# Optimization experiments

Measured on AMD Instinct MI355X. Metric: run time of the kernel, lower is better.

## Reference

```python
import jax, jax.numpy as jnp
import numpy as np

WH, WW = 7, 7            # window size
NUM_HEADS = 4
PROMPT_LEN = 20          # PERTASK_LEN(5) * 4 tasks
DIM = 128
HEAD_DIM = DIM // NUM_HEADS
SCALE = HEAD_DIM ** -0.5


def _relative_position_index(wh, ww):
    coords = np.stack(np.meshgrid(np.arange(wh), np.arange(ww), indexing='ij'))  # [2,wh,ww]
    cf = coords.reshape(2, -1)                               # [2, wh*ww]
    rc = (cf[:, :, None] - cf[:, None, :]).transpose(1, 2, 0).astype(np.int64)
    rc[..., 0] += wh - 1
    rc[..., 1] += ww - 1
    rc[..., 0] *= 2 * ww - 1
    return rc.sum(-1)                                        # [wh*ww, wh*ww]

_REL_IDX = jnp.asarray(_relative_position_index(WH, WW))


def setup_inputs() -> dict:
    key = jax.random.key(0)
    ks = jax.random.split(key, 8)
    B, nW = 32, 64
    B_ = B * nW
    Nw = WH * WW
    return {
        'x': jax.random.normal(ks[0], (B_, Nw, DIM), jnp.float32),
        'spa_prompts': jax.random.normal(ks[1], (B, PROMPT_LEN, DIM), jnp.float32),
        'mask': jax.random.normal(ks[2], (nW, Nw, Nw), jnp.float32),
        'rel_bias_table': jax.random.normal(ks[3], ((2 * WH - 1) * (2 * WW - 1), NUM_HEADS), jnp.float32) * 0.02,
        'W_qkv': jax.random.normal(ks[4], (DIM, 3 * DIM), jnp.float32) * 0.02,
        'b_qkv': jax.random.normal(ks[5], (3 * DIM,), jnp.float32) * 0.02,
        'W_proj': jax.random.normal(ks[6], (DIM, DIM), jnp.float32) * 0.02,
        'b_proj': jax.random.normal(ks[7], (DIM,), jnp.float32) * 0.02,
    }


def reference(x, spa_prompts, mask, rel_bias_table, W_qkv, b_qkv, W_proj, b_proj):
    B_, Nw, C = x.shape
    B = spa_prompts.shape[0]
    nW = B_ // B
    P = PROMPT_LEN
    H = NUM_HEADS

    # replicate prompts per window and concat in front of window tokens
    prompts = jnp.broadcast_to(spa_prompts[:, None], (B, nW, P, C)).reshape(B_, P, C)
    xc = jnp.concatenate([prompts, x], axis=1)               # [B_, N, C]
    N = P + Nw

    qkv = xc @ W_qkv + b_qkv                                 # [B_, N, 3C]
    qkv = qkv.reshape(B_, N, 3, H, HEAD_DIM).transpose(2, 0, 3, 1, 4)
    q, k, v = qkv[0], qkv[1], qkv[2]                         # [B_, H, N, hd]

    attn_w = jnp.einsum('bhnd,bhmd->bhnm', q, k)             # unscaled q@k^T
    attn = attn_w * SCALE

    # relative position bias on the window-token sub-block
    bias = rel_bias_table[_REL_IDX]                          # [Nw, Nw, H]
    bias = bias.transpose(2, 0, 1)                           # [H, Nw, Nw]
    attn = attn.at[:, :, P:, P:].add(bias[None])

    # shifted-window mask on the same sub-block
    attn = attn.reshape(B, nW, H, N, N)
    attn = attn.at[:, :, :, P:, P:].add(mask[None, :, None])
    attn = attn.reshape(B_, H, N, N)

    attn = jax.nn.softmax(attn, axis=-1)

    out = jnp.einsum('bhnm,bhmd->bhnd', attn, v)             # [B_, H, N, hd]
    out = out.transpose(0, 2, 1, 3).reshape(B_, N, C)
    out = out @ W_proj + b_proj

    prompts_out, x_out = out[:, :P, :], out[:, P:, :]
    prompts_out = prompts_out.reshape(B, nW, P, C).mean(axis=1)
    ori_attn_weight = attn_w[:, :, :P, P:]                   # prompt->token raw scores
    return x_out, ori_attn_weight, prompts_out
```

## Files before the change

### kernel.cpp

```cpp
#include <hip/hip_runtime.h>
#include <hip/hip_bf16.h>

#define B_TOT   2048
#define BGRP    32
#define NW      64
#define NWIN    49
#define PLEN    20
#define NTOK    69
#define CDIM    128
#define NH      4
#define HD      32
#define SCALE_F 0.17677669529663687f

#define WIN_ROWS (B_TOT * NWIN)
#define PROMPT_ROWS (BGRP * PLEN)
#define TOT_ROWS (WIN_ROWS + PROMPT_ROWS)
#define PROJ_ROWS (B_TOT * NTOK)

typedef unsigned short ushort_t;
typedef __attribute__((ext_vector_type(8))) short bf16x8;
typedef __attribute__((ext_vector_type(4))) float f32x4;

__device__ __forceinline__ ushort_t f2b(float f) {
    union { float f; unsigned u; } v; v.f = f;
    unsigned r = v.u + 0x7FFFu + ((v.u >> 16) & 1u);
    return (ushort_t)(r >> 16);
}

__global__ __launch_bounds__(256) void convw_kernel(
    const float* __restrict__ Wqkv, const float* __restrict__ Wproj,
    ushort_t* __restrict__ Wtq, ushort_t* __restrict__ Wtp)
{
    int idx = blockIdx.x * 256 + threadIdx.x;
    if (idx < 384 * 128) {
        int n = idx >> 7, k = idx & 127;
        Wtq[idx] = f2b(Wqkv[k * 384 + n]);
    } else {
        int i = idx - 384 * 128;
        int n = i >> 7, k = i & 127;
        Wtp[i] = f2b(Wproj[k * 128 + n]);
    }
}

__global__ __launch_bounds__(256) void bm_kernel(
    const float* __restrict__ relb, const float* __restrict__ mask, float* __restrict__ bm)
{
    int idx = blockIdx.x * 256 + threadIdx.x;
    int jj = idx % 49; int t = idx / 49; int ii = t % 49; int wh = t / 49;
    int h = wh & 3, w = wh >> 2;
    int ridx = (ii / 7 - jj / 7 + 6) * 13 + (ii % 7 - jj % 7 + 6);
    bm[idx] = relb[ridx * NH + h] + mask[((size_t)w * 49 + ii) * 49 + jj];
}

__global__ __launch_bounds__(256) void qkv_kernel(
    const float* __restrict__ x, const float* __restrict__ prompts,
    const ushort_t* __restrict__ Wtq, const float* __restrict__ bqkv,
    ushort_t* __restrict__ q_win, ushort_t* __restrict__ k_win, ushort_t* __restrict__ v_win,
    ushort_t* __restrict__ q_p, ushort_t* __restrict__ k_p, ushort_t* __restrict__ v_p)
{
    __shared__ __align__(16) ushort_t As[128][136];
    __shared__ __align__(16) ushort_t Bs[128][136];
    const int m0 = blockIdx.x * 128;
    const int by = blockIdx.y;
    const int tid = threadIdx.x;

    for (int it = tid; it < 128 * 16; it += 256) {
        int r = it >> 4, ch = it & 15;
        int row = m0 + r;
        const float* src = (row < WIN_ROWS) ? x + (size_t)row * CDIM + ch * 8
                                            : prompts + (size_t)(row - WIN_ROWS) * CDIM + ch * 8;
        float4 v0 = *(const float4*)src;
        float4 v1 = *(const float4*)(src + 4);
        ushort_t tmp[8] = {f2b(v0.x), f2b(v0.y), f2b(v0.z), f2b(v0.w),
                           f2b(v1.x), f2b(v1.y), f2b(v1.z), f2b(v1.w)};
        *(uint4*)&As[r][ch * 8] = *(uint4*)tmp;
    }
    for (int it = tid; it < 128 * 16; it += 256) {
        int r = it >> 4, ch = it & 15;
        *(uint4*)&Bs[r][ch * 8] = *(const uint4*)(Wtq + ((size_t)(by * 128 + r)) * 128 + ch * 8);
    }
    __syncthreads();

    const int lane = tid & 63, wv = tid >> 6;
    const int wr = wv >> 1, wc = wv & 1;
    const int c = lane & 15, quad = lane >> 4;

    f32x4 acc[4][4];
#pragma unroll
    for (int i = 0; i < 4; i++)
#pragma unroll
        for (int j = 0; j < 4; j++) acc[i][j] = (f32x4){0.f, 0.f, 0.f, 0.f};

#pragma unroll
    for (int kc = 0; kc < 4; kc++) {
        bf16x8 a[4], b[4];
#pragma unroll
        for (int i = 0; i < 4; i++) a[i] = *(const bf16x8*)&As[wr * 64 + i * 16 + c][kc * 32 + quad * 8];
#pragma unroll
        for (int j = 0; j < 4; j++) b[j] = *(const bf16x8*)&Bs[wc * 64 + j * 16 + c][kc * 32 + quad * 8];
#pragma unroll
        for (int i = 0; i < 4; i++)
#pragma unroll
            for (int j = 0; j < 4; j++)
                acc[i][j] = __builtin_amdgcn_mfma_f32_16x16x32_bf16(a[i], b[j], acc[i][j], 0, 0, 0);
    }

    ushort_t* dw = (by == 0) ? q_win : (by == 1) ? k_win : v_win;
    ushort_t* dp = (by == 0) ? q_p   : (by == 1) ? k_p   : v_p;
    const bool iswin = (m0 < WIN_ROWS);

#pragma unroll
    for (int j = 0; j < 4; j++) {
        int col = wc * 64 + j * 16 + c;
        float bias = bqkv[by * 128 + col];
        int h = col >> 5, d = col & 31;
#pragma unroll
        for (int i = 0; i < 4; i++) {
            int row0 = m0 + wr * 64 + i * 16 + quad * 4;
            if (iswin) {
                int bidx = row0 / 49, n = row0 - bidx * 49;
#pragma unroll
                for (int rr = 0; rr < 4; rr++) {
                    dw[(((size_t)bidx * NH + h) * NWIN + n) * HD + d] = f2b(acc[i][j][rr] + bias);
                    if (++n == 49) { n = 0; ++bidx; }
                }
            } else {
                int ir = row0 - WIN_ROWS;
                int bb2 = ir / 20, p = ir - bb2 * 20;
#pragma unroll
                for (int rr = 0; rr < 4; rr++) {
                    dp[(((size_t)bb2 * NH + h) * PLEN + p) * HD + d] = f2b(acc[i][j][rr] + bias);
                    if (++p == 20) { p = 0; ++bb2; }
                }
            }
        }
    }
}

__global__ __launch_bounds__(256) void attn_kernel(
    const ushort_t* __restrict__ q_win, const ushort_t* __restrict__ k_win, const ushort_t* __restrict__ v_win,
    const ushort_t* __restrict__ q_p, const ushort_t* __restrict__ k_p, const ushort_t* __restrict__ v_p,
    const float* __restrict__ bm,
    ushort_t* __restrict__ attn_out, float* __restrict__ ori_w)
{
    __shared__ __align__(16) ushort_t Qs[80][72];
    __shared__ __align__(16) ushort_t Ks[80][72];
    __shared__ __align__(16) ushort_t Vt[32][112];
    __shared__ __align__(16) ushort_t Ps[80][104];

    const int b = blockIdx.x >> 2;
    const int h = blockIdx.x & 3;
    const int bb = b >> 6;
    const int w = b & 63;
    const int tid = threadIdx.x;

    for (int it = tid; it < 69 * 4; it += 256) {
        int n = it >> 2, ch = it & 3;
        size_t o;
        const ushort_t *qb, *kb, *vb;
        if (n < PLEN) {
            o = (((size_t)bb * NH + h) * PLEN + n) * HD + ch * 8;
            qb = q_p; kb = k_p; vb = v_p;
        } else {
            o = (((size_t)b * NH + h) * NWIN + (n - PLEN)) * HD + ch * 8;
            qb = q_win; kb = k_win; vb = v_win;
        }
        *(uint4*)&Qs[n][ch * 8] = *(const uint4*)(qb + o);
        *(uint4*)&Ks[n][ch * 8] = *(const uint4*)(kb + o);
        uint4 vv = *(const uint4*)(vb + o);
        ushort_t tmp[8]; *(uint4*)tmp = vv;
#pragma unroll
        for (int d = 0; d < 8; d++) Vt[ch * 8 + d][n] = tmp[d];
    }
    for (int it = tid; it < 11 * 9 * 2; it += 256) {
        int which = it / 99, rem = it % 99;
        int r = 69 + rem / 9, ch = rem % 9;
        uint4 z = {0u, 0u, 0u, 0u};
        if (which == 0) *(uint4*)&Qs[r][ch * 8] = z;
        else            *(uint4*)&Ks[r][ch * 8] = z;
    }
    for (int it = tid; it < 32 * 27; it += 256) Vt[it / 27][69 + it % 27] = 0;
    for (int it = tid; it < 80 * 2; it += 256) {
        uint4 z = {0u, 0u, 0u, 0u};
        *(uint4*)&Ps[it >> 1][80 + (it & 1) * 8] = z;
    }
    __syncthreads();

    const int lane = tid & 63, wv = tid >> 6;
    const int c = lane & 15, quad = lane >> 4;
    const float* bmw = bm + (size_t)(w * NH + h) * (49 * 49);
    float* OtF = (float*)&Qs[0][0];

    for (int itile = wv; itile < 5; itile += 4) {
        bf16x8 aq = *(const bf16x8*)&Qs[itile * 16 + c][quad * 8];
        f32x4 s[5];
#pragma unroll
        for (int j = 0; j < 5; j++) {
            bf16x8 bk = *(const bf16x8*)&Ks[j * 16 + c][quad * 8];
            s[j] = __builtin_amdgcn_mfma_f32_16x16x32_bf16(aq, bk, (f32x4){0.f, 0.f, 0.f, 0.f}, 0, 0, 0);
        }
        const int mbase = itile * 16 + quad * 4;

        if (mbase < 20) {
#pragma unroll
            for (int j = 1; j < 5; j++) {
                int col = j * 16 + c;
                if (col >= 20 && col < 69) {
#pragma unroll
                    for (int rr = 0; rr < 4; rr++) {
                        int m = mbase + rr;
                        if (m < 20)
                            ori_w[(((size_t)b * NH + h) * PLEN + m) * NWIN + (col - 20)] = s[j][rr];
                    }
                }
            }
        }
#pragma unroll
        for (int j = 0; j < 5; j++) {
            int col = j * 16 + c;
#pragma unroll
            for (int rr = 0; rr < 4; rr++) {
                int m = mbase + rr;
                float v;
                if (col >= 69) v = -1e30f;
                else {
                    v = s[j][rr] * SCALE_F;
                    if (m >= 20 && m < 69 && col >= 20)
                        v += bmw[(m - 20) * 49 + (col - 20)];
                }
                s[j][rr] = v;
            }
        }
#pragma unroll
        for (int rr = 0; rr < 4; rr++) {
            float mx = s[0][rr];
#pragma unroll
            for (int j = 1; j < 5; j++) mx = fmaxf(mx, s[j][rr]);
            mx = fmaxf(mx, __shfl_xor(mx, 1));
            mx = fmaxf(mx, __shfl_xor(mx, 2));
            mx = fmaxf(mx, __shfl_xor(mx, 4));
            mx = fmaxf(mx, __shfl_xor(mx, 8));
            float e[5], sum = 0.f;
#pragma unroll
            for (int j = 0; j < 5; j++) { e[j] = __expf(s[j][rr] - mx); sum += e[j]; }
            sum += __shfl_xor(sum, 1);
            sum += __shfl_xor(sum, 2);
            sum += __shfl_xor(sum, 4);
            sum += __shfl_xor(sum, 8);
            float inv = 1.f / sum;
            int m = mbase + rr;
#pragma unroll
            for (int j = 0; j < 5; j++) Ps[m][j * 16 + c] = f2b(e[j] * inv);
        }
#pragma unroll
        for (int dt = 0; dt < 2; dt++) {
            f32x4 o = {0.f, 0.f, 0.f, 0.f};
#pragma unroll
            for (int kc = 0; kc < 3; kc++) {
                bf16x8 pa = *(const bf16x8*)&Ps[itile * 16 + c][kc * 32 + quad * 8];
                bf16x8 vb = *(const bf16x8*)&Vt[dt * 16 + c][kc * 32 + quad * 8];
                o = __builtin_amdgcn_mfma_f32_16x16x32_bf16(pa, vb, o, 0, 0, 0);
            }
#pragma unroll
            for (int rr = 0; rr < 4; rr++)
                OtF[(itile * 16 + quad * 4 + rr) * 36 + dt * 16 + c] = o[rr];
        }
    }
    __syncthreads();

    for (int it = tid; it < 69 * 8; it += 256) {
        int n = it >> 3, ch = it & 7;
        float4 ov = *(const float4*)&OtF[n * 36 + ch * 4];
        uint2 pk;
        pk.x = (unsigned)f2b(ov.x) | ((unsigned)f2b(ov.y) << 16);
        pk.y = (unsigned)f2b(ov.z) | ((unsigned)f2b(ov.w) << 16);
        *(uint2*)(attn_out + ((size_t)b * NTOK + n) * CDIM + h * HD + ch * 4) = pk;
    }
}

__global__ __launch_bounds__(256) void proj_kernel(
    const ushort_t* __restrict__ attn_out, const ushort_t* __restrict__ Wtp,
    const float* __restrict__ bproj,
    float* __restrict__ x_out, float* __restrict__ promptproj)
{
    __shared__ __align__(16) ushort_t As[128][136];
    __shared__ __align__(16) ushort_t Bs[128][136];
    const int m0 = blockIdx.x * 128;
    const int tid = threadIdx.x;

    for (int it = tid; it < 128 * 16; it += 256) {
        int r = it >> 4, ch = it & 15;
        *(uint4*)&As[r][ch * 8] = *(const uint4*)(attn_out + (size_t)(m0 + r) * CDIM + ch * 8);
    }
    for (int it = tid; it < 128 * 16; it += 256) {
        int r = it >> 4, ch = it & 15;
        *(uint4*)&Bs[r][ch * 8] = *(const uint4*)(Wtp + (size_t)r * 128 + ch * 8);
    }
    __syncthreads();

    const int lane = tid & 63, wv = tid >> 6;
    const int wr = wv >> 1, wc = wv & 1;
    const int c = lane & 15, quad = lane >> 4;

    f32x4 acc[4][4];
#pragma unroll
    for (int i = 0; i < 4; i++)
#pragma unroll
        for (int j = 0; j < 4; j++) acc[i][j] = (f32x4){0.f, 0.f, 0.f, 0.f};

#pragma unroll
    for (int kc = 0; kc < 4; kc++) {
        bf16x8 a[4], b[4];
#pragma unroll
        for (int i = 0; i < 4; i++) a[i] = *(const bf16x8*)&As[wr * 64 + i * 16 + c][kc * 32 + quad * 8];
#pragma unroll
        for (int j = 0; j < 4; j++) b[j] = *(const bf16x8*)&Bs[wc * 64 + j * 16 + c][kc * 32 + quad * 8];
#pragma unroll
        for (int i = 0; i < 4; i++)
#pragma unroll
            for (int j = 0; j < 4; j++)
                acc[i][j] = __builtin_amdgcn_mfma_f32_16x16x32_bf16(a[i], b[j], acc[i][j], 0, 0, 0);
    }

#pragma unroll
    for (int j = 0; j < 4; j++) {
        int col = wc * 64 + j * 16 + c;
        float bias = bproj[col];
#pragma unroll
        for (int i = 0; i < 4; i++) {
            int row0 = m0 + wr * 64 + i * 16 + quad * 4;
            int bidx = row0 / 69, n = row0 - bidx * 69;
#pragma unroll
            for (int rr = 0; rr < 4; rr++) {
                float val = acc[i][j][rr] + bias;
                if (n >= PLEN)
                    x_out[((size_t)bidx * NWIN + (n - PLEN)) * CDIM + col] = val;
                else
                    promptproj[((size_t)bidx * PLEN + n) * CDIM + col] = val;
                if (++n == 69) { n = 0; ++bidx; }
            }
        }
    }
}

__global__ __launch_bounds__(256) void mean_kernel(
    const float* __restrict__ promptproj, float* __restrict__ prompts_out)
{
    int idx = blockIdx.x * 256 + threadIdx.x;
    if (idx >= BGRP * PLEN * CDIM) return;
    int c = idx & 127;
    int p = (idx >> 7) % PLEN;
    int bb = idx / (PLEN * CDIM);
    size_t base = (((size_t)bb * NW) * PLEN + p) * CDIM + c;
    float s = 0.f;
    for (int w = 0; w < NW; w++) s += promptproj[base + (size_t)w * (PLEN * CDIM)];
    prompts_out[idx] = s * (1.f / 64.f);
}

extern "C" void kernel_launch(void* const* d_in, const int* in_sizes, int n_in,
                              void* d_out, int out_size, void* d_ws, size_t ws_size,
                              hipStream_t stream)
{
    const float* x       = (const float*)d_in[0];
    const float* prompts = (const float*)d_in[1];
    const float* mask    = (const float*)d_in[2];
    const float* relb    = (const float*)d_in[3];
    const float* Wqkv    = (const float*)d_in[4];
    const float* bqkv    = (const float*)d_in[5];
    const float* Wproj   = (const float*)d_in[6];
    const float* bproj   = (const float*)d_in[7];

    float* out = (float*)d_out;
    float* x_out       = out;
    float* ori_w       = out + (size_t)B_TOT * NWIN * CDIM;
    float* prompts_out = ori_w + (size_t)B_TOT * NH * PLEN * NWIN;

    char* wsb = (char*)d_ws;
    size_t off = 0;
    const size_t winQKV = (size_t)B_TOT * NH * NWIN * HD;
    const size_t pQKV   = (size_t)BGRP * NH * PLEN * HD;
    ushort_t* q_win = (ushort_t*)(wsb + off); off += winQKV * 2;
    ushort_t* k_win = (ushort_t*)(wsb + off); off += winQKV * 2;
    ushort_t* v_win = (ushort_t*)(wsb + off); off += winQKV * 2;
    ushort_t* q_p   = (ushort_t*)(wsb + off); off += pQKV * 2;
    ushort_t* k_p   = (ushort_t*)(wsb + off); off += pQKV * 2;
    ushort_t* v_p   = (ushort_t*)(wsb + off); off += pQKV * 2;
    ushort_t* attn_o = (ushort_t*)(wsb + off); off += (size_t)B_TOT * NTOK * CDIM * 2;
    float* promptproj = (float*)(wsb + off); off += (size_t)B_TOT * PLEN * CDIM * 4;
    float* bm = (float*)(wsb + off); off += (size_t)NW * NH * 49 * 49 * 4;
    ushort_t* Wtq = (ushort_t*)(wsb + off); off += 384 * 128 * 2;
    ushort_t* Wtp = (ushort_t*)(wsb + off); off += 128 * 128 * 2;

    convw_kernel<<<256, 256, 0, stream>>>(Wqkv, Wproj, Wtq, Wtp);
    bm_kernel<<<(NW * NH * 49 * 49) / 256, 256, 0, stream>>>(relb, mask, bm);
    qkv_kernel<<<dim3(TOT_ROWS / 128, 3), 256, 0, stream>>>(x, prompts, Wtq, bqkv,
                                                            q_win, k_win, v_win, q_p, k_p, v_p);
    attn_kernel<<<B_TOT * NH, 256, 0, stream>>>(q_win, k_win, v_win, q_p, k_p, v_p,
                                                bm, attn_o, ori_w);
    proj_kernel<<<PROJ_ROWS / 128, 256, 0, stream>>>(attn_o, Wtp, bproj, x_out, promptproj);
    mean_kernel<<<(BGRP * PLEN * CDIM + 255) / 256, 256, 0, stream>>>(promptproj, prompts_out);
}
```

Before: 306.2 us.

## Use token-major QKV layout, one block per window, and LDS-staged coalesced epilogues

The QKV GEMM now writes q/k/v in token-major [row][128] layout by staging its bf16 output tile in LDS and emitting 16-byte coalesced stores, replacing scattered per-element head-major writes. The attention kernel switches from one block per (window, head) to one block per window, with each wave handling one head. K and Q fragments are loaded straight from global into registers, and V is transposed once into LDS for all heads. The projection epilogue likewise stages fp32 results in LDS for vectorized float4 stores. This targets uncoalesced global writes and redundant loads, at the cost of each wave processing all five query tiles serially and more direct global reads inside the loop.

```diff
diff --git a/kernel.cpp b/kernel.cpp
--- a/kernel.cpp
+++ b/kernel.cpp
@@ -105,100 +105,99 @@
                 acc[i][j] = __builtin_amdgcn_mfma_f32_16x16x32_bf16(a[i], b[j], acc[i][j], 0, 0, 0);
     }
 
-    ushort_t* dw = (by == 0) ? q_win : (by == 1) ? k_win : v_win;
-    ushort_t* dp = (by == 0) ? q_p   : (by == 1) ? k_p   : v_p;
-    const bool iswin = (m0 < WIN_ROWS);
-
+    __syncthreads();
+    ushort_t* Os = &As[0][0];
 #pragma unroll
     for (int j = 0; j < 4; j++) {
         int col = wc * 64 + j * 16 + c;
         float bias = bqkv[by * 128 + col];
-        int h = col >> 5, d = col & 31;
 #pragma unroll
         for (int i = 0; i < 4; i++) {
-            int row0 = m0 + wr * 64 + i * 16 + quad * 4;
-            if (iswin) {
-                int bidx = row0 / 49, n = row0 - bidx * 49;
-#pragma unroll
-                for (int rr = 0; rr < 4; rr++) {
-                    dw[(((size_t)bidx * NH + h) * NWIN + n) * HD + d] = f2b(acc[i][j][rr] + bias);
-                    if (++n == 49) { n = 0; ++bidx; }
-                }
-            } else {
-                int ir = row0 - WIN_ROWS;
-                int bb2 = ir / 20, p = ir - bb2 * 20;
-#pragma unroll
-                for (int rr = 0; rr < 4; rr++) {
-                    dp[(((size_t)bb2 * NH + h) * PLEN + p) * HD + d] = f2b(acc[i][j][rr] + bias);
-                    if (++p == 20) { p = 0; ++bb2; }
-                }
-            }
-        }
-    }
-}
-
-__global__ __launch_bounds__(256) void attn_kernel(
+            int rl = wr * 64 + i * 16 + quad * 4;
+#pragma unroll
+            for (int rr = 0; rr < 4; rr++)
+                Os[(rl + rr) * 136 + col] = f2b(acc[i][j][rr] + bias);
+        }
+    }
+    __syncthreads();
+
+    ushort_t* dw = (by == 0) ? q_win : (by == 1) ? k_win : v_win;
+    ushort_t* dp = (by == 0) ? q_p   : (by == 1) ? k_p   : v_p;
+    for (int it = tid; it < 128 * 16; it += 256) {
+        int r = it >> 4, ch = it & 15;
+        int row = m0 + r;
+        uint4 val = *(uint4*)&Os[r * 136 + ch * 8];
+        if (row < WIN_ROWS) *(uint4*)&dw[(size_t)row * CDIM + ch * 8] = val;
+        else                *(uint4*)&dp[(size_t)(row - WIN_ROWS) * CDIM + ch * 8] = val;
+    }
+}
+
+__global__ __launch_bounds__(256, 3) void attn_kernel(
     const ushort_t* __restrict__ q_win, const ushort_t* __restrict__ k_win, const ushort_t* __restrict__ v_win,
     const ushort_t* __restrict__ q_p, const ushort_t* __restrict__ k_p, const ushort_t* __restrict__ v_p,
     const float* __restrict__ bm,
     ushort_t* __restrict__ attn_out, float* __restrict__ ori_w)
 {
-    __shared__ __align__(16) ushort_t Qs[80][72];
-    __shared__ __align__(16) ushort_t Ks[80][72];
-    __shared__ __align__(16) ushort_t Vt[32][112];
-    __shared__ __align__(16) ushort_t Ps[80][104];
-
-    const int b = blockIdx.x >> 2;
-    const int h = blockIdx.x & 3;
+    __shared__ __align__(16) ushort_t Vt[4][32][104];
+    __shared__ __align__(16) ushort_t Ps[4][16][104];
+
+    const int b = blockIdx.x;
     const int bb = b >> 6;
     const int w = b & 63;
     const int tid = threadIdx.x;
 
-    for (int it = tid; it < 69 * 4; it += 256) {
-        int n = it >> 2, ch = it & 3;
-        size_t o;
-        const ushort_t *qb, *kb, *vb;
-        if (n < PLEN) {
-            o = (((size_t)bb * NH + h) * PLEN + n) * HD + ch * 8;
-            qb = q_p; kb = k_p; vb = v_p;
-        } else {
-            o = (((size_t)b * NH + h) * NWIN + (n - PLEN)) * HD + ch * 8;
-            qb = q_win; kb = k_win; vb = v_win;
-        }
-        *(uint4*)&Qs[n][ch * 8] = *(const uint4*)(qb + o);
-        *(uint4*)&Ks[n][ch * 8] = *(const uint4*)(kb + o);
-        uint4 vv = *(const uint4*)(vb + o);
+    for (int it = tid; it < 64 * 2; it += 256) {
+        int row = it >> 1, half = it & 1;
+        *(uint4*)&Ps[row >> 4][row & 15][80 + half * 8] = (uint4){0u, 0u, 0u, 0u};
+    }
+    for (int it = tid; it < 128 * 27; it += 256) {
+        int d = it / 27, cc = 69 + it % 27;
+        Vt[d >> 5][d & 31][cc] = 0;
+    }
+    for (int it = tid; it < 69 * 16; it += 256) {
+        int n = it >> 4, ch = it & 15;
+        const ushort_t* vb = (n < PLEN) ? v_p + ((size_t)bb * PLEN + n) * CDIM
+                                        : v_win + ((size_t)b * NWIN + (n - PLEN)) * CDIM;
+        uint4 vv = *(const uint4*)(vb + ch * 8);
         ushort_t tmp[8]; *(uint4*)tmp = vv;
-#pragma unroll
-        for (int d = 0; d < 8; d++) Vt[ch * 8 + d][n] = tmp[d];
-    }
-    for (int it = tid; it < 11 * 9 * 2; it += 256) {
-        int which = it / 99, rem = it % 99;
-        int r = 69 + rem / 9, ch = rem % 9;
-        uint4 z = {0u, 0u, 0u, 0u};
-        if (which == 0) *(uint4*)&Qs[r][ch * 8] = z;
-        else            *(uint4*)&Ks[r][ch * 8] = z;
-    }
-    for (int it = tid; it < 32 * 27; it += 256) Vt[it / 27][69 + it % 27] = 0;
-    for (int it = tid; it < 80 * 2; it += 256) {
-        uint4 z = {0u, 0u, 0u, 0u};
-        *(uint4*)&Ps[it >> 1][80 + (it & 1) * 8] = z;
-    }
-    __syncthreads();
-
-    const int lane = tid & 63, wv = tid >> 6;
+        int hh = ch >> 2, dbase = (ch & 3) * 8;
+#pragma unroll
+        for (int i = 0; i < 8; i++) Vt[hh][dbase + i][n] = tmp[i];
+    }
+    __syncthreads();
+
+    const int lane = tid & 63, h = tid >> 6;
     const int c = lane & 15, quad = lane >> 4;
+    const int dsl = h * HD + quad * 8;
+
+    bf16x8 kf[5];
+#pragma unroll
+    for (int j = 0; j < 5; j++) {
+        int n = j * 16 + c; if (n > 68) n = 68;
+        const ushort_t* kb = (n < PLEN) ? k_p + ((size_t)bb * PLEN + n) * CDIM
+                                        : k_win + ((size_t)b * NWIN + (n - PLEN)) * CDIM;
+        kf[j] = *(const bf16x8*)(kb + dsl);
+    }
+    bf16x8 vf[2][3];
+#pragma unroll
+    for (int dt = 0; dt < 2; dt++)
+#pragma unroll
+        for (int kc = 0; kc < 3; kc++)
+            vf[dt][kc] = *(const bf16x8*)&Vt[h][dt * 16 + c][kc * 32 + quad * 8];
+
     const float* bmw = bm + (size_t)(w * NH + h) * (49 * 49);
-    float* OtF = (float*)&Qs[0][0];
-
-    for (int itile = wv; itile < 5; itile += 4) {
-        bf16x8 aq = *(const bf16x8*)&Qs[itile * 16 + c][quad * 8];
+
+    for (int itile = 0; itile < 5; itile++) {
+        int nq = itile * 16 + c; if (nq > 68) nq = 68;
+        const ushort_t* qb = (nq < PLEN) ? q_p + ((size_t)bb * PLEN + nq) * CDIM
+                                         : q_win + ((size_t)b * NWIN + (nq - PLEN)) * CDIM;
+        bf16x8 qf = *(const bf16x8*)(qb + dsl);
+
         f32x4 s[5];
 #pragma unroll
-        for (int j = 0; j < 5; j++) {
-            bf16x8 bk = *(const bf16x8*)&Ks[j * 16 + c][quad * 8];
-            s[j] = __builtin_amdgcn_mfma_f32_16x16x32_bf16(aq, bk, (f32x4){0.f, 0.f, 0.f, 0.f}, 0, 0, 0);
-        }
+        for (int j = 0; j < 5; j++)
+            s[j] = __builtin_amdgcn_mfma_f32_16x16x32_bf16(qf, kf[j], (f32x4){0.f, 0.f, 0.f, 0.f}, 0, 0, 0);
+
         const int mbase = itile * 16 + quad * 4;
 
         if (mbase < 20) {
@@ -233,48 +232,41 @@
         }
 #pragma unroll
         for (int rr = 0; rr < 4; rr++) {
-            float mx = s[0][rr];
-#pragma unroll
-            for (int j = 1; j < 5; j++) mx = fmaxf(mx, s[j][rr]);
+            float mx = fmaxf(fmaxf(fmaxf(s[0][rr], s[1][rr]), fmaxf(s[2][rr], s[3][rr])), s[4][rr]);
             mx = fmaxf(mx, __shfl_xor(mx, 1));
             mx = fmaxf(mx, __shfl_xor(mx, 2));
             mx = fmaxf(mx, __shfl_xor(mx, 4));
             mx = fmaxf(mx, __shfl_xor(mx, 8));
-            float e[5], sum = 0.f;
-#pragma unroll
-            for (int j = 0; j < 5; j++) { e[j] = __expf(s[j][rr] - mx); sum += e[j]; }
+            float e0 = __expf(s[0][rr] - mx), e1 = __expf(s[1][rr] - mx), e2 = __expf(s[2][rr] - mx);
+            float e3 = __expf(s[3][rr] - mx), e4 = __expf(s[4][rr] - mx);
+            float sum = e0 + e1 + e2 + e3 + e4;
             sum += __shfl_xor(sum, 1);
             sum += __shfl_xor(sum, 2);
             sum += __shfl_xor(sum, 4);
             sum += __shfl_xor(sum, 8);
             float inv = 1.f / sum;
-            int m = mbase + rr;
-#pragma unroll
-            for (int j = 0; j < 5; j++) Ps[m][j * 16 + c] = f2b(e[j] * inv);
+            int mrow = quad * 4 + rr;
+            Ps[h][mrow][c]      = f2b(e0 * inv);
+            Ps[h][mrow][16 + c] = f2b(e1 * inv);
+            Ps[h][mrow][32 + c] = f2b(e2 * inv);
+            Ps[h][mrow][48 + c] = f2b(e3 * inv);
+            Ps[h][mrow][64 + c] = f2b(e4 * inv);
         }
 #pragma unroll
         for (int dt = 0; dt < 2; dt++) {
             f32x4 o = {0.f, 0.f, 0.f, 0.f};
 #pragma unroll
             for (int kc = 0; kc < 3; kc++) {
-                bf16x8 pa = *(const bf16x8*)&Ps[itile * 16 + c][kc * 32 + quad * 8];
-                bf16x8 vb = *(const bf16x8*)&Vt[dt * 16 + c][kc * 32 + quad * 8];
-                o = __builtin_amdgcn_mfma_f32_16x16x32_bf16(pa, vb, o, 0, 0, 0);
+                bf16x8 pa = *(const bf16x8*)&Ps[h][c][kc * 32 + quad * 8];
+                o = __builtin_amdgcn_mfma_f32_16x16x32_bf16(pa, vf[dt][kc], o, 0, 0, 0);
             }
 #pragma unroll
-            for (int rr = 0; rr < 4; rr++)
-                OtF[(itile * 16 + quad * 4 + rr) * 36 + dt * 16 + c] = o[rr];
-        }
-    }
-    __syncthreads();
-
-    for (int it = tid; it < 69 * 8; it += 256) {
-        int n = it >> 3, ch = it & 7;
-        float4 ov = *(const float4*)&OtF[n * 36 + ch * 4];
-        uint2 pk;
-        pk.x = (unsigned)f2b(ov.x) | ((unsigned)f2b(ov.y) << 16);
-        pk.y = (unsigned)f2b(ov.z) | ((unsigned)f2b(ov.w) << 16);
-        *(uint2*)(attn_out + ((size_t)b * NTOK + n) * CDIM + h * HD + ch * 4) = pk;
+            for (int rr = 0; rr < 4; rr++) {
+                int m = mbase + rr;
+                if (m < 69)
+                    attn_out[((size_t)b * NTOK + m) * CDIM + h * HD + dt * 16 + c] = f2b(o[rr]);
+            }
+        }
     }
 }
 
@@ -283,8 +275,11 @@
     const float* __restrict__ bproj,
     float* __restrict__ x_out, float* __restrict__ promptproj)
 {
-    __shared__ __align__(16) ushort_t As[128][136];
-    __shared__ __align__(16) ushort_t Bs[128][136];
+    __shared__ __align__(16) char smem[128 * 136 * 4];
+    ushort_t (*As)[136] = (ushort_t(*)[136])smem;
+    ushort_t (*Bs)[136] = (ushort_t(*)[136])(smem + 128 * 136 * 2);
+    float (*Osf)[136] = (float(*)[136])smem;
+
     const int m0 = blockIdx.x * 128;
     const int tid = threadIdx.x;
 
@@ -322,24 +317,30 @@
                 acc[i][j] = __builtin_amdgcn_mfma_f32_16x16x32_bf16(a[i], b[j], acc[i][j], 0, 0, 0);
     }
 
+    __syncthreads();
 #pragma unroll
     for (int j = 0; j < 4; j++) {
         int col = wc * 64 + j * 16 + c;
         float bias = bproj[col];
 #pragma unroll
         for (int i = 0; i < 4; i++) {
-            int row0 = m0 + wr * 64 + i * 16 + quad * 4;
-            int bidx = row0 / 69, n = row0 - bidx * 69;
-#pragma unroll
-            for (int rr = 0; rr < 4; rr++) {
-                float val = acc[i][j][rr] + bias;
-                if (n >= PLEN)
-                    x_out[((size_t)bidx * NWIN + (n - PLEN)) * CDIM + col] = val;
-                else
-                    promptproj[((size_t)bidx * PLEN + n) * CDIM + col] = val;
-                if (++n == 69) { n = 0; ++bidx; }
-            }
-        }
+            int rl = wr * 64 + i * 16 + quad * 4;
+#pragma unroll
+            for (int rr = 0; rr < 4; rr++)
+                Osf[rl + rr][col] = acc[i][j][rr] + bias;
+        }
+    }
+    __syncthreads();
+
+    for (int it = tid; it < 128 * 32; it += 256) {
+        int r = it >> 5, ch = it & 31;
+        float4 val = *(float4*)&Osf[r][ch * 4];
+        int row = m0 + r;
+        int bidx = row / NTOK, n = row - bidx * NTOK;
+        if (n >= PLEN)
+            *(float4*)&x_out[((size_t)bidx * NWIN + (n - PLEN)) * CDIM + ch * 4] = val;
+        else
+            *(float4*)&promptproj[((size_t)bidx * PLEN + n) * CDIM + ch * 4] = val;
     }
 }
 
@@ -377,15 +378,15 @@
 
     char* wsb = (char*)d_ws;
     size_t off = 0;
-    const size_t winQKV = (size_t)B_TOT * NH * NWIN * HD;
-    const size_t pQKV   = (size_t)BGRP * NH * PLEN * HD;
+    const size_t winQKV = (size_t)WIN_ROWS * CDIM;
+    const size_t pQKV   = (size_t)PROMPT_ROWS * CDIM;
     ushort_t* q_win = (ushort_t*)(wsb + off); off += winQKV * 2;
     ushort_t* k_win = (ushort_t*)(wsb + off); off += winQKV * 2;
     ushort_t* v_win = (ushort_t*)(wsb + off); off += winQKV * 2;
     ushort_t* q_p   = (ushort_t*)(wsb + off); off += pQKV * 2;
     ushort_t* k_p   = (ushort_t*)(wsb + off); off += pQKV * 2;
     ushort_t* v_p   = (ushort_t*)(wsb + off); off += pQKV * 2;
-    ushort_t* attn_o = (ushort_t*)(wsb + off); off += (size_t)B_TOT * NTOK * CDIM * 2;
+    ushort_t* attn_o = (ushort_t*)(wsb + off); off += (size_t)PROJ_ROWS * CDIM * 2;
     float* promptproj = (float*)(wsb + off); off += (size_t)B_TOT * PLEN * CDIM * 4;
     float* bm = (float*)(wsb + off); off += (size_t)NW * NH * 49 * 49 * 4;
     ushort_t* Wtq = (ushort_t*)(wsb + off); off += 384 * 128 * 2;
@@ -395,8 +396,8 @@
     bm_kernel<<<(NW * NH * 49 * 49) / 256, 256, 0, stream>>>(relb, mask, bm);
     qkv_kernel<<<dim3(TOT_ROWS / 128, 3), 256, 0, stream>>>(x, prompts, Wtq, bqkv,
                                                             q_win, k_win, v_win, q_p, k_p, v_p);
-    attn_kernel<<<B_TOT * NH, 256, 0, stream>>>(q_win, k_win, v_win, q_p, k_p, v_p,
-                                                bm, attn_o, ori_w);
+    attn_kernel<<<B_TOT, 256, 0, stream>>>(q_win, k_win, v_win, q_p, k_p, v_p,
+                                           bm, attn_o, ori_w);
     proj_kernel<<<PROJ_ROWS / 128, 256, 0, stream>>>(attn_o, Wtp, bproj, x_out, promptproj);
     mean_kernel<<<(BGRP * PLEN * CDIM + 255) / 256, 256, 0, stream>>>(promptproj, prompts_out);
 }
```

Result: faster. 269.7 us (-11.9%).
